# Kernel optimization log

Hardware: AMD Instinct MI355X
Metric: run time of the kernel (lower is better)

## Reference

```python
import jax, jax.numpy as jnp
import numpy as np

K = 20
EPS = 1e-5
NEG_SLOPE = 0.2


def knn_idx(pts, k):
    # pts: [B, N, C] -> indices of k nearest neighbors [B, N, k]
    sq = jnp.sum(pts * pts, axis=-1)                     # [B, N]
    inner = jnp.einsum('bnc,bmc->bnm', pts, pts)         # [B, N, N]
    dist = sq[:, :, None] - 2.0 * inner + sq[:, None, :] # [B, N, N]
    _, idx = jax.lax.top_k(-dist, k)                     # nearest = smallest dist
    return idx


def batchnorm(h, gamma, beta):
    # h: [B, N, k, C]; normalize over (B, N, k) per channel (training-mode stats)
    mean = jnp.mean(h, axis=(0, 1, 2), keepdims=True)
    var = jnp.var(h, axis=(0, 1, 2), keepdims=True)
    return gamma * (h - mean) * jax.lax.rsqrt(var + EPS) + beta


def setup_inputs() -> dict:
    key = jax.random.key(0)
    ks = jax.random.split(key, 7)
    B, C, N = 8, 3, 4096
    x = jax.random.normal(ks[0], (B, C, N), dtype=jnp.float32)
    W1 = jax.random.normal(ks[1], (64, 6), dtype=jnp.float32) * (1.0 / np.sqrt(6.0))
    gamma1 = jnp.ones((64,), dtype=jnp.float32)
    beta1 = jnp.zeros((64,), dtype=jnp.float32)
    W2 = jax.random.normal(ks[2], (64, 64), dtype=jnp.float32) * (1.0 / 8.0)
    gamma2 = jnp.ones((64,), dtype=jnp.float32)
    beta2 = jnp.zeros((64,), dtype=jnp.float32)
    return {"x": x, "W1": W1, "gamma1": gamma1, "beta1": beta1,
            "W2": W2, "gamma2": gamma2, "beta2": beta2}


def reference(x, W1, gamma1, beta1, W2, gamma2, beta2):
    # x: [B, 3, N] point cloud
    pts = jnp.transpose(x, (0, 2, 1))                    # [B, N, 3]
    idx = knn_idx(pts, K)                                # [B, N, k]
    nbr = jax.vmap(lambda p, i: p[i])(pts, idx)          # [B, N, k, 3]
    center = pts[:, :, None, :]                          # [B, N, 1, 3]
    edge = jnp.concatenate(
        [nbr - center, jnp.broadcast_to(center, nbr.shape)], axis=-1)  # [B, N, k, 6]

    h = jnp.einsum('bnkc,oc->bnko', edge, W1)            # [B, N, k, 64]
    h = jax.nn.leaky_relu(batchnorm(h, gamma1, beta1), NEG_SLOPE)
    h = jnp.einsum('bnkc,oc->bnko', h, W2)               # [B, N, k, 64]
    h = jax.nn.leaky_relu(batchnorm(h, gamma2, beta2), NEG_SLOPE)

    out = jnp.max(h, axis=2)                             # max-pool over k neighbors
    return jnp.transpose(out, (0, 2, 1))                 # [B, 64, N]
```

## Files before the change

kernel.cpp:

```cpp
#include <hip/hip_runtime.h>
#include <hip/hip_bf16.h>
#include <math.h>

#define BB 8
#define NN 4096
#define KNN 20
#define CH 64
#define SAMPLES (BB*NN*KNN)
#define EPSF 1e-5f
#define SLOPE 0.2f
#define MCOPY 32

typedef float f32x4 __attribute__((ext_vector_type(4)));
typedef short bf16x8 __attribute__((ext_vector_type(8)));

__device__ __forceinline__ float key_decode(unsigned e) {
    return __uint_as_float((e & 0x80000000u) ? (e ^ 0x80000000u) : ~e);
}

__device__ __forceinline__ void rank_flush(unsigned long long* ovf,
                                           unsigned long long* inc,
                                           unsigned long long* scr,
                                           int& cnt, float& kthd, int lane) {
    while (cnt > 0) {
        int take = cnt < 44 ? cnt : 44;
        unsigned long long key;
        if (lane < take)      key = ovf[cnt - take + lane];
        else if (lane >= 44)  key = inc[lane - 44];
        else                  key = ~0ull;
        scr[lane] = key;
        __builtin_amdgcn_wave_barrier();
        int r = 0;
#pragma unroll
        for (int t = 0; t < 64; ++t) {
            unsigned long long kt = scr[t];
            r += (kt < key) ? 1 : 0;
        }
        __builtin_amdgcn_wave_barrier();
        if (r < KNN) inc[r] = key;
        __builtin_amdgcn_wave_barrier();
        kthd = key_decode((unsigned)(inc[KNN-1] >> 32));
        cnt -= take;
    }
}

__global__ __launch_bounds__(1024) void sort_kernel(const float* __restrict__ x,
        float4* __restrict__ pts4, float4* __restrict__ sp4, int* __restrict__ sidx,
        int* __restrict__ rankArr, double* __restrict__ zreg) {
#pragma clang fp contract(off)
    __shared__ unsigned long long S[NN];
    const int tid = threadIdx.x;
    const int b = blockIdx.x;
    if (b == 0 && tid < 992) zreg[tid] = 0.0;
    const float* xb = x + (size_t)b * 3 * NN;
    for (int i = tid; i < NN; i += 1024) {
        float mx = xb[i], my = xb[NN + i], mz = xb[2*NN + i];
        float sq = mx*mx; sq += my*my; sq += mz*mz;
        pts4[(b << 12) + i] = make_float4(-2.0f*mx, -2.0f*my, -2.0f*mz, sq);
        unsigned uu = __float_as_uint(mx);
        unsigned e = uu ^ (((unsigned)((int)uu >> 31)) | 0x80000000u);
        S[i] = ((unsigned long long)e << 32) | (unsigned)i;
    }
    __syncthreads();
    for (int k = 2; k <= NN; k <<= 1) {
        for (int j = k >> 1; j > 0; j >>= 1) {
#pragma unroll
            for (int tt = 0; tt < 2; ++tt) {
                int t = tid + tt*1024;
                int i = ((t & ~(j - 1)) << 1) | (t & (j - 1));
                int h = i | j;
                unsigned long long a = S[i], c = S[h];
                bool up = ((i & k) == 0);
                if ((a > c) == up) { S[i] = c; S[h] = a; }
            }
            __syncthreads();
        }
    }
    for (int s = tid; s < NN; s += 1024) {
        int oi = (int)(unsigned)(S[s] & 0xFFFFFFFFu);
        float mx = xb[oi], my = xb[NN + oi], mz = xb[2*NN + oi];
        float sq = mx*mx; sq += my*my; sq += mz*mz;
        sp4[(b << 12) + s] = make_float4(-2.0f*mx, -2.0f*my, -2.0f*mz, sq);
        sidx[(b << 12) + s] = oi;
        rankArr[(b << 12) + oi] = s;
    }
}

__global__ __launch_bounds__(256) void knn_kernel(const float4* __restrict__ pts4,
        const float4* __restrict__ sp4, const int* __restrict__ sidx,
        int* __restrict__ idx_out, double* __restrict__ mstats) {
#pragma clang fp contract(off)
    __shared__ unsigned long long OVF[4][296];
    __shared__ unsigned long long INC[4][24];
    __shared__ unsigned long long SCR[4][64];
    __shared__ float MOM[4][27];
    const int tid = threadIdx.x;
    const int lane = tid & 63;
    const int wv = __builtin_amdgcn_readfirstlane(tid >> 6);
    const int s = blockIdx.x * 4 + wv;
    const int b = s >> 12;
    const int ss = s & (NN - 1);
    const float4* sb = sp4 + ((size_t)b << 12);
    const int* si = sidx + ((size_t)b << 12);
    unsigned long long* ovf = &OVF[wv][0];
    unsigned long long* inc = &INC[wv][0];
    unsigned long long* scr = &SCR[wv][0];

    const float4 Qc = sb[ss];
    const float qx = -0.5f*Qc.x, qy = -0.5f*Qc.y, qz = -0.5f*Qc.z;
    const float sqn = Qc.w;
    int c0 = ss - 32; c0 = c0 < 0 ? 0 : (c0 > NN-64 ? NN-64 : c0);
    float kthd, thr, M;
    int cnt = 0;

    {
        const float4 P = sb[c0 + lane];
        const float mx = -0.5f*P.x, my = -0.5f*P.y, mz = -0.5f*P.z;
        float inner = qx*mx; inner += qy*my; inner += qz*mz;
        const float d = (sqn - 2.0f*inner) + P.w;
        unsigned uu = __float_as_uint(d);
        unsigned e = uu ^ (((unsigned)((int)uu >> 31)) | 0x80000000u);
        unsigned long long key = ((unsigned long long)e << 32) | (unsigned)si[c0 + lane];
        scr[lane] = key;
        __builtin_amdgcn_wave_barrier();
        int r = 0;
#pragma unroll
        for (int t = 0; t < 64; ++t) {
            unsigned long long kt = scr[t];
            r += (kt < key) ? 1 : 0;
        }
        __builtin_amdgcn_wave_barrier();
        if (r < KNN) inc[r] = key;
        __builtin_amdgcn_wave_barrier();
        kthd = key_decode((unsigned)(inc[KNN-1] >> 32));
        M = 1e-3f*(fabsf(kthd) + fabsf(sqn) + 1.0f);
        thr = (kthd - sqn) + M;
    }

    int lo = c0, hi = c0 + 64;
    bool dl = (lo == 0), dr = (hi == NN);

    float4 PL0, PL1, PR0, PR1;
    float xL = 0.f, xR = 0.f;
    if (!dl) {
        int base = lo - 128; base = base < 0 ? 0 : base;
        PL0 = sb[base + lane];
        PL1 = sb[base + 64 + lane];
        xL = sb[lo - 1].x;
    }
    if (!dr) {
        int s0 = hi + lane;      int a0 = s0 < NN-1 ? s0 : NN-1;
        int s1 = hi + 64 + lane; int a1 = s1 < NN-1 ? s1 : NN-1;
        PR0 = sb[a0]; PR1 = sb[a1];
        xR = sb[hi].x;
    }

    while (!dl || !dr) {
        bool goL = false, goR = false;
        if (!dl) {
            const float dx = qx - (-0.5f*xL);
            goL = (dx*dx <= kthd + M);
            if (!goL) dl = true;
        }
        if (!dr) {
            const float dx = (-0.5f*xR) - qx;
            goR = (dx*dx <= kthd + M);
            if (!goR) dr = true;
        }
        const int baseL = (lo - 128) < 0 ? 0 : (lo - 128);
        const int enR   = (hi + 128) > NN ? NN : (hi + 128);

        float4 PL0n = PL0, PL1n = PL1, PR0n = PR0, PR1n = PR1;
        float xLn = 0.f, xRn = 0.f;
        if (goL && baseL > 0) {
            int b2 = baseL - 128; b2 = b2 < 0 ? 0 : b2;
            PL0n = sb[b2 + lane];
            PL1n = sb[b2 + 64 + lane];
            xLn = sb[baseL - 1].x;
        }
        if (goR && enR < NN) {
            int s0 = enR + lane;      int a0 = s0 < NN-1 ? s0 : NN-1;
            int s1 = enR + 64 + lane; int a1 = s1 < NN-1 ? s1 : NN-1;
            PR0n = sb[a0]; PR1n = sb[a1];
            xRn = sb[enR].x;
        }

        if (cnt > 32) {
            rank_flush(ovf, inc, scr, cnt, kthd, lane);
            M = 1e-3f*(fabsf(kthd) + fabsf(sqn) + 1.0f);
            thr = (kthd - sqn) + M;
        }

        if (goL) {
#pragma unroll
            for (int j = 0; j < 2; ++j) {
                const float4 P = (j == 0) ? PL0 : PL1;
                const int sI = baseL + j*64 + lane;
                const bool valid = sI < lo;
                const float sc = fmaf(P.x, qx, fmaf(P.y, qy, fmaf(P.z, qz, P.w)));
                bool push = valid && (sc <= thr);
                unsigned long long mask = __ballot(push);
                if (mask) {
                    if (push) {
                        const float mx = -0.5f*P.x, my = -0.5f*P.y, mz = -0.5f*P.z;
                        float inner = qx*mx; inner += qy*my; inner += qz*mz;
                        const float d = (sqn - 2.0f*inner) + P.w;
                        unsigned uu = __float_as_uint(d);
                        unsigned e = uu ^ (((unsigned)((int)uu >> 31)) | 0x80000000u);
                        unsigned long long key = ((unsigned long long)e << 32) | (unsigned)si[sI];
                        int ofs = (int)__popcll(mask & ((1ull << lane) - 1ull));
                        ovf[cnt + ofs] = key;
                    }
                    cnt += (int)__popcll(mask);
                }
            }
            lo = baseL;
            dl = (lo == 0);
            PL0 = PL0n; PL1 = PL1n; xL = xLn;
        }
        if (goR) {
#pragma unroll
            for (int j = 0; j < 2; ++j) {
                const float4 P = (j == 0) ? PR0 : PR1;
                const int sI = hi + j*64 + lane;
                const bool valid = sI < enR;
                const float sc = fmaf(P.x, qx, fmaf(P.y, qy, fmaf(P.z, qz, P.w)));
                bool push = valid && (sc <= thr);
                unsigned long long mask = __ballot(push);
                if (mask) {
                    if (push) {
                        const float mx = -0.5f*P.x, my = -0.5f*P.y, mz = -0.5f*P.z;
                        float inner = qx*mx; inner += qy*my; inner += qz*mz;
                        const float d = (sqn - 2.0f*inner) + P.w;
                        unsigned uu = __float_as_uint(d);
                        unsigned e = uu ^ (((unsigned)((int)uu >> 31)) | 0x80000000u);
                        unsigned long long key = ((unsigned long long)e << 32) | (unsigned)si[sI];
                        int ofs = (int)__popcll(mask & ((1ull << lane) - 1ull));
                        ovf[cnt + ofs] = key;
                    }
                    cnt += (int)__popcll(mask);
                }
            }
            hi = enR;
            dr = (hi == NN);
            PR0 = PR0n; PR1 = PR1n; xR = xRn;
        }
    }
    rank_flush(ovf, inc, scr, cnt, kthd, lane);

    if (lane < KNN)
        idx_out[(size_t)s * KNN + lane] = (int)(unsigned)(inc[lane] & 0xFFFFFFFFull);

    float nx = 0.f, ny = 0.f, nz = 0.f, xx = 0.f, xy = 0.f, xz = 0.f,
          yy = 0.f, yz = 0.f, zz = 0.f;
    if (lane < KNN) {
        int nbr = (int)(unsigned)(inc[lane] & 0xFFFFFFFFull);
        float4 pn = pts4[(b << 12) + nbr];
        nx = -0.5f*pn.x; ny = -0.5f*pn.y; nz = -0.5f*pn.z;
        xx = nx*nx; xy = nx*ny; xz = nx*nz; yy = ny*ny; yz = ny*nz; zz = nz*nz;
    }
#pragma unroll
    for (int off = 16; off > 0; off >>= 1) {
        nx += __shfl_xor(nx, off); ny += __shfl_xor(ny, off); nz += __shfl_xor(nz, off);
        xx += __shfl_xor(xx, off); xy += __shfl_xor(xy, off); xz += __shfl_xor(xz, off);
        yy += __shfl_xor(yy, off); yz += __shfl_xor(yz, off); zz += __shfl_xor(zz, off);
    }
    if (lane == 0) {
        MOM[wv][0] = nx;  MOM[wv][1] = ny;  MOM[wv][2] = nz;
        MOM[wv][3] = qx;  MOM[wv][4] = qy;  MOM[wv][5] = qz;
        MOM[wv][6] = xx;  MOM[wv][7] = xy;  MOM[wv][8] = xz;
        MOM[wv][9] = yy;  MOM[wv][10] = yz; MOM[wv][11] = zz;
        MOM[wv][12] = nx*qx; MOM[wv][13] = nx*qy; MOM[wv][14] = nx*qz;
        MOM[wv][15] = ny*qx; MOM[wv][16] = ny*qy; MOM[wv][17] = ny*qz;
        MOM[wv][18] = nz*qx; MOM[wv][19] = nz*qy; MOM[wv][20] = nz*qz;
        MOM[wv][21] = qx*qx; MOM[wv][22] = qx*qy; MOM[wv][23] = qx*qz;
        MOM[wv][24] = qy*qy; MOM[wv][25] = qy*qz; MOM[wv][26] = qz*qz;
    }
    __syncthreads();
    if (tid < 27)
        atomicAdd(&mstats[(blockIdx.x & (MCOPY-1))*27 + tid],
                  (double)(MOM[0][tid] + MOM[1][tid] + MOM[2][tid] + MOM[3][tid]));
}

__device__ __forceinline__ void bsplit(float g, short& hi, short& lo) {
    unsigned bits = __float_as_uint(g);
    unsigned hbits = bits & 0xFFFF0000u;
    float rem = g - __uint_as_float(hbits);
    hi = (short)(bits >> 16);
    lo = (short)(__float_as_uint(rem) >> 16);
}

__global__ __launch_bounds__(256, 2) void main_kernel(const int* __restrict__ idxb,
        const int* __restrict__ rankArr, const float4* __restrict__ pts4,
        const double* __restrict__ ms, const float* __restrict__ W1,
        const float* __restrict__ gamma1, const float* __restrict__ beta1,
        const float* __restrict__ W2,
        float* __restrict__ maxbuf, float* __restrict__ stats2f) {
    __shared__ __align__(16) short Thi[4][32*72];
    __shared__ __align__(16) short Tlo[4][32*72];
    __shared__ float chs[128];
    __shared__ float ab1s[128];
    __shared__ double msd[27];
    const int tid = threadIdx.x;
    const int lane = tid & 63;
    const int wv = __builtin_amdgcn_readfirstlane(tid >> 6);
    const int l15 = lane & 15;
    const int quad = lane >> 4;
    if (tid < 128) chs[tid] = 0.f;
    if (tid < 27) {
        double t = 0.0;
        for (int c = 0; c < MCOPY; ++c) t += ms[c*27 + tid];
        msd[tid] = t;
    }
    __syncthreads();
    if (tid < 64) {
        int c = tid;
        double wu[3], wvv[3];
#pragma unroll
        for (int i = 0; i < 3; ++i) {
            wu[i] = (double)W1[c*6 + i];
            wvv[i] = (double)W1[c*6 + 3 + i] - wu[i];
        }
        const double S = (double)SAMPLES;
        double mean = (wu[0]*msd[0] + wu[1]*msd[1] + wu[2]*msd[2]
                     + 20.0*(wvv[0]*msd[3] + wvv[1]*msd[4] + wvv[2]*msd[5])) / S;
        double qM1 = wu[0]*wu[0]*msd[6] + wu[1]*wu[1]*msd[9] + wu[2]*wu[2]*msd[11]
                   + 2.0*(wu[0]*wu[1]*msd[7] + wu[0]*wu[2]*msd[8] + wu[1]*wu[2]*msd[10]);
        double cross = 0.0;
#pragma unroll
        for (int i = 0; i < 3; ++i)
#pragma unroll
            for (int j = 0; j < 3; ++j)
                cross += wu[i] * msd[12 + i*3 + j] * wvv[j];
        double qpp = wvv[0]*wvv[0]*msd[21] + wvv[1]*wvv[1]*msd[24] + wvv[2]*wvv[2]*msd[26]
                   + 2.0*(wvv[0]*wvv[1]*msd[22] + wvv[0]*wvv[2]*msd[23] + wvv[1]*wvv[2]*msd[25]);
        double e2 = (qM1 + 2.0*cross + 20.0*qpp) / S;
        double var = e2 - mean*mean;
        float a = (float)((double)gamma1[c] / sqrt(var + (double)EPSF));
        ab1s[c] = a;
        ab1s[64 + c] = beta1[c] - a * (float)mean;
    }
    __syncthreads();

    bf16x8 whi[8], wlo[8];
#pragma unroll
    for (int t = 0; t < 4; ++t)
#pragma unroll
    for (int f = 0; f < 2; ++f) {
        const int o = 16*t + l15;
        const int c0 = 32*f + quad*8;
        const float4* wr = (const float4*)(W2 + o*64 + c0);
        float4 w0 = wr[0], w1 = wr[1];
        float vals[8] = {w0.x,w0.y,w0.z,w0.w,w1.x,w1.y,w1.z,w1.w};
        bf16x8 h, l;
#pragma unroll
        for (int j = 0; j < 8; ++j) { short hj, lj; bsplit(vals[j], hj, lj); h[j]=hj; l[j]=lj; }
        whi[t*2+f] = h; wlo[t*2+f] = l;
    }

    const float w10 = W1[lane*6+0], w11 = W1[lane*6+1], w12 = W1[lane*6+2];
    const float w13 = W1[lane*6+3], w14 = W1[lane*6+4], w15 = W1[lane*6+5];
    const float a1 = ab1s[lane], b1 = ab1s[64 + lane];
    float ssum[4] = {0.f,0.f,0.f,0.f}, ssq[4] = {0.f,0.f,0.f,0.f};
    float lm[4][4];
    short* thi = &Thi[wv][0];
    short* tlo = &Tlo[wv][0];

    const int pt0 = (blockIdx.x * 4 + wv) * 4;
    const int b = pt0 >> 12;
    const float4* pb = pts4 + ((size_t)b << 12);
    const int* rnk = rankArr + ((size_t)b << 12);

    for (int p = 0; p < 4; ++p) {
        const int pt = pt0 + p;
        const float4 pc = pb[pt & (NN - 1)];
        const float X = -0.5f*pc.x, Y = -0.5f*pc.y, Z = -0.5f*pc.z;
        const float vc = (w13 - w10)*X + (w14 - w11)*Y + (w15 - w12)*Z;
        const int srow = rnk[pt & (NN - 1)];
        const int* irow = idxb + ((size_t)((b << 12) + srow)) * KNN;

        int nidx[KNN];
#pragma unroll
        for (int k = 0; k < KNN; ++k) nidx[k] = irow[k];
        float4 nbr[KNN];
#pragma unroll
        for (int k = 0; k < KNN; ++k) nbr[k] = pb[nidx[k]];
#pragma unroll
        for (int k = 0; k < KNN; ++k) {
            const float4 pn = nbr[k];
            float nx = -0.5f*pn.x, ny = -0.5f*pn.y, nz = -0.5f*pn.z;
            float uc = w10*nx + w11*ny + w12*nz;
            float g = a1 * (uc + vc) + b1;
            g = fmaxf(g, SLOPE * g);
            short hj, lj; bsplit(g, hj, lj);
            const int row = (k < 16) ? k : (16 + p*4 + (k - 16));
            thi[row*72 + lane] = hj;
            tlo[row*72 + lane] = lj;
        }
        __builtin_amdgcn_wave_barrier();

        bf16x8 ah1[2], al1[2];
#pragma unroll
        for (int f = 0; f < 2; ++f) {
            const int co = 32*f + quad*8;
            ah1[f] = *(const bf16x8*)&thi[l15*72 + co];
            al1[f] = *(const bf16x8*)&tlo[l15*72 + co];
        }

        f32x4 acc1[4];
#pragma unroll
        for (int t = 0; t < 4; ++t) acc1[t] = (f32x4)0.f;
#pragma unroll
        for (int t = 0; t < 4; ++t) {
#pragma unroll
            for (int f = 0; f < 2; ++f) {
                acc1[t] = __builtin_amdgcn_mfma_f32_16x16x32_bf16(ah1[f], whi[t*2+f], acc1[t], 0,0,0);
                acc1[t] = __builtin_amdgcn_mfma_f32_16x16x32_bf16(al1[f], whi[t*2+f], acc1[t], 0,0,0);
                acc1[t] = __builtin_amdgcn_mfma_f32_16x16x32_bf16(ah1[f], wlo[t*2+f], acc1[t], 0,0,0);
            }
        }
        __builtin_amdgcn_wave_barrier();

#pragma unroll
        for (int t = 0; t < 4; ++t) {
            float m1 = fmaxf(fmaxf(acc1[t][0], acc1[t][1]), fmaxf(acc1[t][2], acc1[t][3]));
            float s1 = acc1[t][0] + acc1[t][1] + acc1[t][2] + acc1[t][3];
            float q1 = acc1[t][0]*acc1[t][0] + acc1[t][1]*acc1[t][1]
                     + acc1[t][2]*acc1[t][2] + acc1[t][3]*acc1[t][3];
            m1 = fmaxf(m1, __shfl_xor(m1, 16)); m1 = fmaxf(m1, __shfl_xor(m1, 32));
            s1 += __shfl_xor(s1, 16); s1 += __shfl_xor(s1, 32);
            q1 += __shfl_xor(q1, 16); q1 += __shfl_xor(q1, 32);
            lm[p][t] = m1;
            ssum[t] += s1; ssq[t] += q1;
        }
    }

    {
        bf16x8 ah2[2], al2[2];
#pragma unroll
        for (int f = 0; f < 2; ++f) {
            const int co = 32*f + quad*8;
            ah2[f] = *(const bf16x8*)&thi[(16 + l15)*72 + co];
            al2[f] = *(const bf16x8*)&tlo[(16 + l15)*72 + co];
        }
        f32x4 accC[4];
#pragma unroll
        for (int t = 0; t < 4; ++t) accC[t] = (f32x4)0.f;
#pragma unroll
        for (int t = 0; t < 4; ++t) {
#pragma unroll
            for (int f = 0; f < 2; ++f) {
                accC[t] = __builtin_amdgcn_mfma_f32_16x16x32_bf16(ah2[f], whi[t*2+f], accC[t], 0,0,0);
                accC[t] = __builtin_amdgcn_mfma_f32_16x16x32_bf16(al2[f], whi[t*2+f], accC[t], 0,0,0);
                accC[t] = __builtin_amdgcn_mfma_f32_16x16x32_bf16(ah2[f], wlo[t*2+f], accC[t], 0,0,0);
            }
        }
#pragma unroll
        for (int t = 0; t < 4; ++t) {
            float cm = fmaxf(fmaxf(accC[t][0], accC[t][1]), fmaxf(accC[t][2], accC[t][3]));
            float cs = accC[t][0] + accC[t][1] + accC[t][2] + accC[t][3];
            float cq = accC[t][0]*accC[t][0] + accC[t][1]*accC[t][1]
                     + accC[t][2]*accC[t][2] + accC[t][3]*accC[t][3];
            float lmq = (quad == 0) ? lm[0][t] : (quad == 1) ? lm[1][t]
                      : (quad == 2) ? lm[2][t] : lm[3][t];
            maxbuf[((size_t)(pt0 + quad) << 6) + 16*t + l15] = fmaxf(lmq, cm);
            cs += __shfl_xor(cs, 16); cs += __shfl_xor(cs, 32);
            cq += __shfl_xor(cq, 16); cq += __shfl_xor(cq, 32);
            ssum[t] += cs; ssq[t] += cq;
        }
    }

    if (quad == 0) {
#pragma unroll
        for (int t = 0; t < 4; ++t) {
            atomicAdd(&chs[16*t + l15], ssum[t]);
            atomicAdd(&chs[64 + 16*t + l15], ssq[t]);
        }
    }
    __syncthreads();
    if (tid < 128)
        atomicAdd(&stats2f[(blockIdx.x & 1)*128 + tid], chs[tid]);
}

__global__ __launch_bounds__(256) void out_kernel(const float* __restrict__ maxbuf,
        const float* __restrict__ s2f, const float* __restrict__ gamma2,
        const float* __restrict__ beta2, float* __restrict__ out) {
    __shared__ float t[64][65];
    __shared__ float ab2s[128];
    const int tid = threadIdx.x;
    if (tid < 64) {
        int o = tid;
        double sum = (double)s2f[o] + (double)s2f[128 + o];
        double sq  = (double)s2f[64 + o] + (double)s2f[192 + o];
        double cnt = (double)SAMPLES;
        double mean = sum / cnt;
        double var  = sq / cnt - mean*mean;
        float a = (float)((double)gamma2[o] / sqrt(var + (double)EPSF));
        ab2s[o] = a;
        ab2s[64 + o] = beta2[o] - a * (float)mean;
    }
    const int b = blockIdx.x >> 6;
    const int n0 = (blockIdx.x & 63) << 6;
#pragma unroll
    for (int i = 0; i < 16; ++i) {
        int r = (tid >> 6) + i*4;
        int c = tid & 63;
        t[r][c] = maxbuf[(((size_t)((b << 12) + n0 + r)) << 6) + c];
    }
    __syncthreads();
#pragma unroll
    for (int i = 0; i < 16; ++i) {
        int o = (tid >> 6) + i*4;
        int nn = tid & 63;
        float a = ab2s[o], bb = ab2s[64 + o];
        float h = a * t[nn][o] + bb;
        out[(((size_t)(b*64 + o)) << 12) + n0 + nn] = h >= 0.f ? h : SLOPE*h;
    }
}

extern "C" void kernel_launch(void* const* d_in, const int* in_sizes, int n_in,
                              void* d_out, int out_size, void* d_ws, size_t ws_size,
                              hipStream_t stream) {
    const float* x      = (const float*)d_in[0];
    const float* W1     = (const float*)d_in[1];
    const float* gamma1 = (const float*)d_in[2];
    const float* beta1  = (const float*)d_in[3];
    const float* W2     = (const float*)d_in[4];
    const float* gamma2 = (const float*)d_in[5];
    const float* beta2  = (const float*)d_in[6];
    float* out = (float*)d_out;

    char* ws = (char*)d_ws;
    int*    idxb    = (int*)   (ws + 0);
    float4* pts4    = (float4*)(ws + 2621440);
    float4* sp4     = (float4*)(ws + 3145728);
    int*    sidx    = (int*)   (ws + 3670016);
    int*    rankArr = (int*)   (ws + 3801088);
    float*  maxbuf  = (float*) (ws + 19398656);
    double* mstats  = (double*)(ws + 27787264);
    float*  stats2f = (float*) (ws + 27794176);
    double* zreg    = (double*)(ws + 27787264);

    sort_kernel <<<8, 1024, 0, stream>>>(x, pts4, sp4, sidx, rankArr, zreg);
    knn_kernel  <<<8192, 256, 0, stream>>>(pts4, sp4, sidx, idxb, mstats);
    main_kernel <<<2048, 256, 0, stream>>>(idxb, rankArr, pts4, mstats, W1, gamma1,
                                           beta1, W2, maxbuf, stats2f);
    out_kernel  <<<512, 256, 0, stream>>>(maxbuf, stats2f, gamma2, beta2, out);
}
```

Before: 254.2 us.

## Replace per-batch bitonic sort with parallel rank-counting sort across 128 blocks

The single-block-per-batch bitonic sort (8 blocks of 1024 threads, many barriers) becomes a rank sort. Each of 16 blocks per batch loads all keys into LDS and computes each point's rank by counting smaller keys. The change spreads work over more CUs and removes the barrier-heavy sort stages. In exchange each block does O(N) comparisons per point and every block reloads the whole batch's keys.

```diff
diff --git a/kernel.cpp b/kernel.cpp
--- a/kernel.cpp
+++ b/kernel.cpp
@@ -44,46 +44,39 @@
     }
 }
 
-__global__ __launch_bounds__(1024) void sort_kernel(const float* __restrict__ x,
+__global__ __launch_bounds__(256) void sort_kernel(const float* __restrict__ x,
         float4* __restrict__ pts4, float4* __restrict__ sp4, int* __restrict__ sidx,
         int* __restrict__ rankArr, double* __restrict__ zreg) {
 #pragma clang fp contract(off)
     __shared__ unsigned long long S[NN];
     const int tid = threadIdx.x;
-    const int b = blockIdx.x;
-    if (b == 0 && tid < 992) zreg[tid] = 0.0;
+    const int b     = blockIdx.x >> 4;
+    const int chunk = blockIdx.x & 15;
+    if (blockIdx.x == 0)
+        for (int z = tid; z < 992; z += 256) zreg[z] = 0.0;
     const float* xb = x + (size_t)b * 3 * NN;
-    for (int i = tid; i < NN; i += 1024) {
-        float mx = xb[i], my = xb[NN + i], mz = xb[2*NN + i];
-        float sq = mx*mx; sq += my*my; sq += mz*mz;
-        pts4[(b << 12) + i] = make_float4(-2.0f*mx, -2.0f*my, -2.0f*mz, sq);
-        unsigned uu = __float_as_uint(mx);
+
+    for (int j = tid; j < NN; j += 256) {
+        unsigned uu = __float_as_uint(xb[j]);
         unsigned e = uu ^ (((unsigned)((int)uu >> 31)) | 0x80000000u);
-        S[i] = ((unsigned long long)e << 32) | (unsigned)i;
+        S[j] = ((unsigned long long)e << 32) | (unsigned)j;
     }
     __syncthreads();
-    for (int k = 2; k <= NN; k <<= 1) {
-        for (int j = k >> 1; j > 0; j >>= 1) {
-#pragma unroll
-            for (int tt = 0; tt < 2; ++tt) {
-                int t = tid + tt*1024;
-                int i = ((t & ~(j - 1)) << 1) | (t & (j - 1));
-                int h = i | j;
-                unsigned long long a = S[i], c = S[h];
-                bool up = ((i & k) == 0);
-                if ((a > c) == up) { S[i] = c; S[h] = a; }
-            }
-            __syncthreads();
-        }
-    }
-    for (int s = tid; s < NN; s += 1024) {
-        int oi = (int)(unsigned)(S[s] & 0xFFFFFFFFu);
-        float mx = xb[oi], my = xb[NN + oi], mz = xb[2*NN + oi];
-        float sq = mx*mx; sq += my*my; sq += mz*mz;
-        sp4[(b << 12) + s] = make_float4(-2.0f*mx, -2.0f*my, -2.0f*mz, sq);
-        sidx[(b << 12) + s] = oi;
-        rankArr[(b << 12) + oi] = s;
-    }
+
+    const int i = (chunk << 8) + tid;
+    const unsigned long long ku = S[i];
+    int r = 0;
+#pragma unroll 8
+    for (int j = 0; j < NN; ++j)
+        r += (S[j] < ku) ? 1 : 0;
+
+    const float mx = xb[i], my = xb[NN + i], mz = xb[2*NN + i];
+    float sq = mx*mx; sq += my*my; sq += mz*mz;
+    const float4 v = make_float4(-2.0f*mx, -2.0f*my, -2.0f*mz, sq);
+    pts4[(b << 12) + i] = v;
+    sp4[(b << 12) + r] = v;
+    sidx[(b << 12) + r] = i;
+    rankArr[(b << 12) + i] = r;
 }
 
 __global__ __launch_bounds__(256) void knn_kernel(const float4* __restrict__ pts4,
@@ -541,7 +534,7 @@
     float*  stats2f = (float*) (ws + 27794176);
     double* zreg    = (double*)(ws + 27787264);
 
-    sort_kernel <<<8, 1024, 0, stream>>>(x, pts4, sp4, sidx, rankArr, zreg);
+    sort_kernel <<<128, 256, 0, stream>>>(x, pts4, sp4, sidx, rankArr, zreg);
     knn_kernel  <<<8192, 256, 0, stream>>>(pts4, sp4, sidx, idxb, mstats);
     main_kernel <<<2048, 256, 0, stream>>>(idxb, rankArr, pts4, mstats, W1, gamma1,
                                            beta1, W2, maxbuf, stats2f);
```

Measured after the change: 274.9 us. 1.08x slower.
